# Kernel optimization log

Measured on AMD Instinct MI355X. Metric: run time of the kernel, lower is better.

The kernel has to match this reference:

```python
import jax, jax.numpy as jnp
import numpy as np
import math

N_OBS, DIM_IN, DIM_HIDDEN = 2048, 64, 1024
LENGTHSCALE = 1.0


def setup_inputs() -> dict:
    key = jax.random.key(0)
    kx, kw, kb = jax.random.split(key, 3)
    x = jax.random.normal(kx, (N_OBS, DIM_IN), dtype=jnp.float32)
    # buffer w ~ Normal(0, 1/lengthscale), b ~ Uniform(0, 2*pi)
    w = jax.random.normal(kw, (DIM_HIDDEN, DIM_IN), dtype=jnp.float32) / LENGTHSCALE
    b = jax.random.uniform(kb, (DIM_HIDDEN,), dtype=jnp.float32, minval=0.0, maxval=2.0 * math.pi)
    return {"x": x, "w": w, "b": b}


def reference(x, w, b):
    """compute_Ax: analytic jacobian of hidden_features + per-dim Gram matrices.

    hidden h = sqrt(2/K) * cos(x @ w.T + b)
    jacobian J[n,k,d] = -sqrt(2/K) * sin(z[n,k]) * w[k,d]
    A_d[k,l] = (1/n) * sum_n J[n,k,d] * J[n,l,d]
             = (1/n) * (S^T S)[k,l] * w[k,d] * w[l,d],  S = -sqrt(2/K) sin(z)
    Returns A stacked: (dim_in, K, K).
    """
    n = x.shape[0]
    K = w.shape[0]
    scale = math.sqrt(2.0 / K)
    z = x @ w.T + b  # (n, K)
    s = (-scale) * jnp.sin(z)  # (n, K)
    M = (s.T @ s) / n  # (K, K) shared Gram of sin-activations
    # A[d,k,l] = M[k,l] * w[k,d] * w[l,d]
    A = jnp.einsum('kl,kd,ld->dkl', M, w, w)
    return A
```

## Files before the change

kernel.cpp:

```cpp
#include <hip/hip_runtime.h>
#include <math.h>

#define N_OBS   2048
#define DIM_IN  64
#define K_HID   1024
#define NCHUNK  (N_OBS / 64)

typedef unsigned short ushort_t;
typedef __attribute__((ext_vector_type(8))) short bf16x8;
typedef __attribute__((ext_vector_type(4))) float f32x4;

__device__ __forceinline__ ushort_t f2bf(float f) {
    unsigned int u = __float_as_uint(f);
    u += 0x7FFF + ((u >> 16) & 1);
    return (ushort_t)(u >> 16);
}

#define GLD_LDS16(g, l)                                                   \
    __builtin_amdgcn_global_load_lds(                                     \
        (const __attribute__((address_space(1))) void*)(g),               \
        (__attribute__((address_space(3))) void*)(l), 16, 0, 0)

__global__ __launch_bounds__(256) void rff_compute_s(
    const float* __restrict__ x, const float* __restrict__ w,
    const float* __restrict__ b, ushort_t* __restrict__ sT) {
    __shared__ float xs[16][64];
    __shared__ float wT[64][65];

    const int t  = threadIdx.x;
    const int k0 = blockIdx.x * 64;
    const int n0 = blockIdx.y * 16;

    {
        int r = t >> 4, c = (t & 15) * 4;
        *(float4*)&xs[r][c] = *(const float4*)(x + (n0 + r) * DIM_IN + c);
    }
#pragma unroll
    for (int i = 0; i < 4; ++i) {
        int r = (t >> 4) + 16 * i, c = (t & 15) * 4;
        float4 v = *(const float4*)(w + (k0 + r) * DIM_IN + c);
        wT[c + 0][r] = v.x; wT[c + 1][r] = v.y;
        wT[c + 2][r] = v.z; wT[c + 3][r] = v.w;
    }
    __syncthreads();

    const int k  = t & 63;
    const int nb = t >> 6;
    const float bk = b[k0 + k];
    float z[4];
#pragma unroll
    for (int i = 0; i < 4; ++i) z[i] = bk;

    for (int d4 = 0; d4 < 64; d4 += 4) {
        float xv[4][4];
#pragma unroll
        for (int i = 0; i < 4; ++i)
            *(float4*)xv[i] = *(const float4*)&xs[nb * 4 + i][d4];
#pragma unroll
        for (int j = 0; j < 4; ++j) {
            const float wv = wT[d4 + j][k];
#pragma unroll
            for (int i = 0; i < 4; ++i) z[i] += xv[i][j] * wv;
        }
    }

    const float scale = 0.04419417382415922f;
    ushort4 ov;
    ov.x = f2bf(-scale * __sinf(z[0]));
    ov.y = f2bf(-scale * __sinf(z[1]));
    ov.z = f2bf(-scale * __sinf(z[2]));
    ov.w = f2bf(-scale * __sinf(z[3]));
    *(ushort4*)(sT + (size_t)(k0 + k) * N_OBS + n0 + nb * 4) = ov;
}

__device__ __forceinline__ void stage_tiles(
    const ushort_t* __restrict__ sT, ushort_t* lA, ushort_t* lB,
    int k0, int l0, int ncol0, int wv, int srow, int sslot) {
#pragma unroll
    for (int j = 0; j < 2; ++j) {
        const int c = wv * 2 + j;
        const ushort_t* gA = sT + (size_t)(k0 + c * 8 + srow) * N_OBS + ncol0 + sslot * 8;
        const ushort_t* gB = sT + (size_t)(l0 + c * 8 + srow) * N_OBS + ncol0 + sslot * 8;
        GLD_LDS16(gA, lA + c * 512);
        GLD_LDS16(gB, lB + c * 512);
    }
}

__global__ __launch_bounds__(256) void rff_gram_expand(
    const ushort_t* __restrict__ sT, const float* __restrict__ w,
    float* __restrict__ out) {
    __shared__ __align__(16) char smem[52224];
    ushort_t* ldsA  = (ushort_t*)smem;
    ushort_t* ldsB  = (ushort_t*)(smem + 16384);
    float*    M_lds = (float*)smem;
    float*    wkT   = (float*)(smem + 17408);
    float*    wlT   = (float*)(smem + 34816);

    const int t    = threadIdx.x;
    const int lane = t & 63;
    const int wv   = t >> 6;
    const int wr   = wv >> 1, wc = wv & 1;
    const int k0   = blockIdx.y * 64, l0 = blockIdx.x * 64;

    const int srow  = lane >> 3;
    const int sslot = (lane & 7) ^ srow;

    f32x4 acc[2][2];
#pragma unroll
    for (int a = 0; a < 2; ++a)
#pragma unroll
        for (int bb = 0; bb < 2; ++bb)
            acc[a][bb] = (f32x4){0.f, 0.f, 0.f, 0.f};

    const int rlo = lane & 15;
    const int hi  = lane >> 4;
    const int rx  = rlo & 7;

    stage_tiles(sT, ldsA, ldsB, k0, l0, 0, wv, srow, sslot);
    __syncthreads();

    int cur = 0;
    for (int it = 0; it < NCHUNK; ++it) {
        if (it + 1 < NCHUNK)
            stage_tiles(sT, ldsA + (cur ^ 1) * 4096, ldsB + (cur ^ 1) * 4096,
                        k0, l0, (it + 1) * 64, wv, srow, sslot);
#pragma unroll
        for (int ks = 0; ks < 2; ++ks) {
            const int slot = (ks * 4 + hi) ^ rx;
            bf16x8 af[2], bfr[2];
#pragma unroll
            for (int a = 0; a < 2; ++a) {
                af[a]  = *(const bf16x8*)(ldsA + cur * 4096
                          + (wr * 32 + a * 16 + rlo) * 64 + slot * 8);
                bfr[a] = *(const bf16x8*)(ldsB + cur * 4096
                          + (wc * 32 + a * 16 + rlo) * 64 + slot * 8);
            }
#pragma unroll
            for (int a = 0; a < 2; ++a)
#pragma unroll
                for (int bb = 0; bb < 2; ++bb)
                    acc[a][bb] = __builtin_amdgcn_mfma_f32_16x16x32_bf16(
                        af[a], bfr[bb], acc[a][bb], 0, 0, 0);
        }
        __syncthreads();
        cur ^= 1;
    }

    const float inv_n = 1.0f / (float)N_OBS;
    const int col = lane & 15;
    const int rq  = (lane >> 4) * 4;
#pragma unroll
    for (int a = 0; a < 2; ++a)
#pragma unroll
        for (int bb = 0; bb < 2; ++bb)
#pragma unroll
            for (int r = 0; r < 4; ++r) {
                const int row = wr * 32 + a * 16 + rq + r;
                const int cl  = wc * 32 + bb * 16 + col;
                M_lds[row * 68 + cl] = acc[a][bb][r] * inv_n;
            }
#pragma unroll
    for (int i = 0; i < 4; ++i) {
        const int r = (t >> 4) + 16 * i, c = (t & 15) * 4;
        float4 vk = *(const float4*)(w + (k0 + r) * DIM_IN + c);
        float4 vl = *(const float4*)(w + (l0 + r) * DIM_IN + c);
        wkT[(c + 0) * 68 + r] = vk.x; wkT[(c + 1) * 68 + r] = vk.y;
        wkT[(c + 2) * 68 + r] = vk.z; wkT[(c + 3) * 68 + r] = vk.w;
        wlT[(c + 0) * 68 + r] = vl.x; wlT[(c + 1) * 68 + r] = vl.y;
        wlT[(c + 2) * 68 + r] = vl.z; wlT[(c + 3) * 68 + r] = vl.w;
    }
    __syncthreads();

    const int prow = t >> 4;
    const int pcol = (t & 15) * 4;
    f32x4 mv[4];
#pragma unroll
    for (int rr = 0; rr < 4; ++rr)
        mv[rr] = *(const f32x4*)&M_lds[(rr * 16 + prow) * 68 + pcol];

    float* outb = out + (size_t)k0 * K_HID + l0;
    for (int d = 0; d < DIM_IN; ++d) {
        const f32x4 wlv = *(const f32x4*)&wlT[d * 68 + pcol];
        float* outd = outb + (size_t)d * K_HID * K_HID;
#pragma unroll
        for (int rr = 0; rr < 4; ++rr) {
            const int row = rr * 16 + prow;
            const float wk = wkT[d * 68 + row];
            f32x4 o;
#pragma unroll
            for (int j = 0; j < 4; ++j) o[j] = mv[rr][j] * wk * wlv[j];
            __builtin_nontemporal_store(
                o, (f32x4*)(outd + (size_t)row * K_HID + pcol));
        }
    }
}

extern "C" void kernel_launch(void* const* d_in, const int* in_sizes, int n_in,
                              void* d_out, int out_size, void* d_ws, size_t ws_size,
                              hipStream_t stream) {
    const float* x = (const float*)d_in[0];
    const float* w = (const float*)d_in[1];
    const float* b = (const float*)d_in[2];
    float* out = (float*)d_out;

    ushort_t* sT_buf = (ushort_t*)d_ws;

    rff_compute_s<<<dim3(K_HID / 64, N_OBS / 16), 256, 0, stream>>>(x, w, b, sT_buf);
    rff_gram_expand<<<dim3(K_HID / 64, K_HID / 64), 256, 0, stream>>>(sT_buf, w, out);
}
```

Before: 296.6 us.

## Triple-buffer Gram staging with single barrier and vmcnt-based waits

Replaces the double-buffered LDS staging in the Gram kernel with a three-stage ring. Each iteration uses explicit vmcnt waits and one barrier instead of two syncthreads, so global-to-LDS loads run two chunks ahead of the MFMA work. The expansion store loop is also unrolled by two. The change relies on manual waitcnt counts matching the number of in-flight loads, which is fragile if the staging pattern changes.

```diff
diff --git a/kernel.cpp b/kernel.cpp
--- a/kernel.cpp
+++ b/kernel.cpp
@@ -74,15 +74,15 @@
 }
 
 __device__ __forceinline__ void stage_tiles(
-    const ushort_t* __restrict__ sT, ushort_t* lA, ushort_t* lB,
+    const ushort_t* __restrict__ sT, ushort_t* buf,
     int k0, int l0, int ncol0, int wv, int srow, int sslot) {
 #pragma unroll
     for (int j = 0; j < 2; ++j) {
         const int c = wv * 2 + j;
         const ushort_t* gA = sT + (size_t)(k0 + c * 8 + srow) * N_OBS + ncol0 + sslot * 8;
         const ushort_t* gB = sT + (size_t)(l0 + c * 8 + srow) * N_OBS + ncol0 + sslot * 8;
-        GLD_LDS16(gA, lA + c * 512);
-        GLD_LDS16(gB, lB + c * 512);
+        GLD_LDS16(gA, buf + c * 512);
+        GLD_LDS16(gB, buf + 4096 + c * 512);
     }
 }
 
@@ -90,8 +90,7 @@
     const ushort_t* __restrict__ sT, const float* __restrict__ w,
     float* __restrict__ out) {
     __shared__ __align__(16) char smem[52224];
-    ushort_t* ldsA  = (ushort_t*)smem;
-    ushort_t* ldsB  = (ushort_t*)(smem + 16384);
+    ushort_t* stg   = (ushort_t*)smem;
     float*    M_lds = (float*)smem;
     float*    wkT   = (float*)(smem + 17408);
     float*    wlT   = (float*)(smem + 34816);
@@ -116,24 +115,29 @@
     const int hi  = lane >> 4;
     const int rx  = rlo & 7;
 
-    stage_tiles(sT, ldsA, ldsB, k0, l0, 0, wv, srow, sslot);
-    __syncthreads();
-
-    int cur = 0;
+    stage_tiles(sT, stg,        k0, l0,  0, wv, srow, sslot);
+    stage_tiles(sT, stg + 8192, k0, l0, 64, wv, srow, sslot);
+
     for (int it = 0; it < NCHUNK; ++it) {
-        if (it + 1 < NCHUNK)
-            stage_tiles(sT, ldsA + (cur ^ 1) * 4096, ldsB + (cur ^ 1) * 4096,
-                        k0, l0, (it + 1) * 64, wv, srow, sslot);
+        if (it == NCHUNK - 1) {
+            asm volatile("s_waitcnt vmcnt(0)" ::: "memory");
+        } else {
+            asm volatile("s_waitcnt vmcnt(4)" ::: "memory");
+        }
+        __builtin_amdgcn_s_barrier();
+        if (it + 2 < NCHUNK)
+            stage_tiles(sT, stg + ((it + 2) % 3) * 8192,
+                        k0, l0, (it + 2) * 64, wv, srow, sslot);
+        const ushort_t* bufA = stg + (it % 3) * 8192;
+        const ushort_t* bufB = bufA + 4096;
 #pragma unroll
         for (int ks = 0; ks < 2; ++ks) {
             const int slot = (ks * 4 + hi) ^ rx;
             bf16x8 af[2], bfr[2];
 #pragma unroll
             for (int a = 0; a < 2; ++a) {
-                af[a]  = *(const bf16x8*)(ldsA + cur * 4096
-                          + (wr * 32 + a * 16 + rlo) * 64 + slot * 8);
-                bfr[a] = *(const bf16x8*)(ldsB + cur * 4096
-                          + (wc * 32 + a * 16 + rlo) * 64 + slot * 8);
+                af[a]  = *(const bf16x8*)(bufA + (wr * 32 + a * 16 + rlo) * 64 + slot * 8);
+                bfr[a] = *(const bf16x8*)(bufB + (wc * 32 + a * 16 + rlo) * 64 + slot * 8);
             }
 #pragma unroll
             for (int a = 0; a < 2; ++a)
@@ -142,9 +146,8 @@
                     acc[a][bb] = __builtin_amdgcn_mfma_f32_16x16x32_bf16(
                         af[a], bfr[bb], acc[a][bb], 0, 0, 0);
         }
-        __syncthreads();
-        cur ^= 1;
-    }
+    }
+    __syncthreads();
 
     const float inv_n = 1.0f / (float)N_OBS;
     const int col = lane & 15;
@@ -179,6 +182,7 @@
         mv[rr] = *(const f32x4*)&M_lds[(rr * 16 + prow) * 68 + pcol];
 
     float* outb = out + (size_t)k0 * K_HID + l0;
+#pragma unroll 2
     for (int d = 0; d < DIM_IN; ++d) {
         const f32x4 wlv = *(const f32x4*)&wlT[d * 68 + pcol];
         float* outd = outb + (size_t)d * K_HID * K_HID;
```

Result: no change. 291.1 us (-1.8%).
